# Kernel tuning notes

Hardware: AMD Instinct MI355X
Metric: run time of the kernel (lower is better)

## Reference

```python
import jax, jax.numpy as jnp
import numpy as np

HEADS = 4
DIM_U = 1
DIM_K = 16
DIM_V = 32  # dim_out // heads = 128 // 4
EPS = 1e-5


def setup_inputs() -> dict:
    key = jax.random.key(0)
    ks = jax.random.split(key, 9)
    b, dim, hh, ww = 16, 256, 32, 32
    n = m = hh * ww
    x = jax.random.normal(ks[0], (b, dim, hh, ww), dtype=jnp.float32)
    # 1x1 conv weights (out_ch, in_ch), kaiming-ish scale
    s = 1.0 / np.sqrt(dim)
    w_q = jax.random.normal(ks[1], (DIM_K * HEADS, dim), dtype=jnp.float32) * s
    w_k = jax.random.normal(ks[2], (DIM_K * DIM_U, dim), dtype=jnp.float32) * s
    w_v = jax.random.normal(ks[3], (DIM_V * DIM_U, dim), dtype=jnp.float32) * s
    pos_emb = jax.random.normal(ks[4], (n, m, DIM_K, DIM_U), dtype=jnp.float32)
    gamma_q = jnp.ones((DIM_K * HEADS,), dtype=jnp.float32)
    beta_q = jnp.zeros((DIM_K * HEADS,), dtype=jnp.float32)
    gamma_v = jnp.ones((DIM_V * DIM_U,), dtype=jnp.float32)
    beta_v = jnp.zeros((DIM_V * DIM_U,), dtype=jnp.float32)
    return {"x": x, "w_q": w_q, "w_k": w_k, "w_v": w_v, "pos_emb": pos_emb,
            "gamma_q": gamma_q, "beta_q": beta_q, "gamma_v": gamma_v, "beta_v": beta_v}


def _bn(t, gamma, beta):
    # BatchNorm2d in training mode: batch statistics over (b, h, w), biased var
    mean = t.mean(axis=(0, 2, 3), keepdims=True)
    var = t.var(axis=(0, 2, 3), keepdims=True)
    t = (t - mean) * jax.lax.rsqrt(var + EPS)
    return t * gamma[None, :, None, None] + beta[None, :, None, None]


def reference(x, w_q, w_k, w_v, pos_emb, gamma_q, beta_q, gamma_v, beta_v):
    b, c, hh, ww = x.shape
    h, u, dk, dv = HEADS, DIM_U, DIM_K, DIM_V
    # 1x1 convs == channel contractions
    q = jnp.einsum('oc,bcxy->boxy', w_q, x)
    k = jnp.einsum('oc,bcxy->boxy', w_k, x)
    v = jnp.einsum('oc,bcxy->boxy', w_v, x)
    q = _bn(q, gamma_q, beta_q)
    v = _bn(v, gamma_v, beta_v)
    n = hh * ww
    q = q.reshape(b, h, dk, n)        # b h k n
    k = k.reshape(b, dk, u, n)        # b k u m
    v = v.reshape(b, dv, u, n)        # b v u m
    k = jax.nn.softmax(k, axis=-1)
    lam_c = jnp.einsum('bkum,bvum->bkv', k, v)            # content lambda
    lam_p = jnp.einsum('nmku,bvum->bnkv', pos_emb, v)     # position lambdas
    Yc = jnp.einsum('bhkn,bkv->bnhv', q, lam_c)
    Yp = jnp.einsum('bhkn,bnkv->bnhv', q, lam_p)
    Y = Yc + Yp                                           # b n h v
    out = Y.transpose(0, 2, 3, 1).reshape(b, h * dv, hh, ww)
    return out
```

## Files before the change

### kernel.cpp

```cpp
#include <hip/hip_runtime.h>
#include <hip/hip_bf16.h>
#include <cstdint>


typedef __attribute__((ext_vector_type(8))) __bf16 bf16x8;
typedef __attribute__((ext_vector_type(4))) float f32x4;

__device__ __forceinline__ unsigned short f2bf(float f) {
    unsigned u = __float_as_uint(f);
    u += 0x7fffu + ((u >> 16) & 1u);
    return (unsigned short)(u >> 16);
}
__device__ __forceinline__ float bf2f(unsigned short h) {
    return __uint_as_float(((unsigned)h) << 16);
}
__device__ __forceinline__ void async16(const void* g, void* l) {
    __builtin_amdgcn_global_load_lds(
        (const __attribute__((address_space(1))) void*)g,
        (__attribute__((address_space(3))) void*)l, 16, 0, 0);
}

__global__ __launch_bounds__(256) void k_transp(const float* __restrict__ pos,
                                                unsigned* __restrict__ PbfU,
                                                const float* __restrict__ wq,
                                                const float* __restrict__ wk,
                                                const float* __restrict__ wv,
                                                unsigned* __restrict__ WbfU) {
    int blk = blockIdx.x;
    int t = threadIdx.x;
    if (blk >= 1024) {
        int tt = (blk - 1024) * 256 + t;
#pragma unroll
        for (int r = 0; r < 4; ++r) {
            int u = r * 4096 + tt;
            int row = u >> 7;
            int cp = (u & 127) << 1;
            float f0 = 0.f, f1 = 0.f;
            if (row < 64)       { f0 = wq[row * 256 + cp];        f1 = wq[row * 256 + cp + 1]; }
            else if (row < 80)  { f0 = wk[(row - 64) * 256 + cp]; f1 = wk[(row - 64) * 256 + cp + 1]; }
            else if (row < 112) { f0 = wv[(row - 80) * 256 + cp]; f1 = wv[(row - 80) * 256 + cp + 1]; }
            WbfU[u] = (unsigned)f2bf(f0) | ((unsigned)f2bf(f1) << 16);
        }
        return;
    }
    __shared__ __align__(16) unsigned short L[16 * 1032];
    const float4* src = (const float4*)(pos + (size_t)blk * 16384);
#pragma unroll
    for (int r = 0; r < 16; ++r) {
        int idx4 = r * 256 + t;
        float4 f = src[idx4];
        int m = idx4 >> 2, k0 = (idx4 & 3) << 2;
        L[(k0 + 0) * 1032 + m] = f2bf(f.x);
        L[(k0 + 1) * 1032 + m] = f2bf(f.y);
        L[(k0 + 2) * 1032 + m] = f2bf(f.z);
        L[(k0 + 3) * 1032 + m] = f2bf(f.w);
    }
    __syncthreads();
    uint2* dst = (uint2*)(PbfU + (size_t)blk * 8192);
#pragma unroll
    for (int r = 0; r < 16; ++r) {
        int c = r * 256 + t;
        int k = c >> 8, mo = c & 255;
        dst[c] = *(const uint2*)&L[k * 1032 + mo * 4];
    }
}

__global__ __launch_bounds__(256) void k_proj(const float* __restrict__ x,
                                              const unsigned short* __restrict__ Wbf,
                                              float* __restrict__ qraw,
                                              float* __restrict__ kraw,
                                              float* __restrict__ vraw) {
    int b = blockIdx.y;
    int px0 = blockIdx.x * 128;
    int t = threadIdx.x;
    int w = t >> 6, lane = t & 63;

    __shared__ __align__(16) unsigned short Al[128 * 32];
    __shared__ __align__(16) unsigned short Bl[128 * 40];

    int srow = (w << 5) + (lane >> 2);
    int schunk = (lane & 3) ^ ((lane >> 3) & 3);
    const unsigned short* pA0 = Wbf + srow * 256 + schunk * 8;
    const unsigned short* pA1 = pA0 + 16 * 256;
    unsigned short* lA0 = &Al[w * 1024];
    unsigned short* lA1 = lA0 + 512;

    int wm = w >> 1, wn = w & 1;
    int rl = lane & 15, qq = lane >> 4;
    int sw = qq ^ ((rl >> 1) & 3);

    f32x4 acc[4][4];
#pragma unroll
    for (int i = 0; i < 4; ++i)
#pragma unroll
        for (int j = 0; j < 4; ++j)
#pragma unroll
            for (int r = 0; r < 4; ++r) acc[i][j][r] = 0.f;

    const float* xb = x + (size_t)b * 256 * 1024 + px0;

    for (int kt = 0; kt < 8; ++kt) {
        int c0 = kt * 32;
        async16(pA0 + c0, lA0);
        async16(pA1 + c0, lA1);
#pragma unroll
        for (int rep = 0; rep < 8; ++rep) {
            int idx = rep * 256 + t;
            int px = idx & 127;
            int cp = idx >> 7;
            int c = c0 + cp * 2;
            float f0 = xb[(size_t)c * 1024 + px];
            float f1 = xb[(size_t)(c + 1) * 1024 + px];
            *(unsigned*)&Bl[px * 40 + cp * 2] = (unsigned)f2bf(f0) | ((unsigned)f2bf(f1) << 16);
        }
        __syncthreads();
        bf16x8 a[4], bb[4];
#pragma unroll
        for (int i = 0; i < 4; ++i) a[i]  = *(const bf16x8*)&Al[((wm << 6) + (i << 4) + rl) * 32 + sw * 8];
#pragma unroll
        for (int j = 0; j < 4; ++j) bb[j] = *(const bf16x8*)&Bl[((wn << 6) + (j << 4) + rl) * 40 + qq * 8];
#pragma unroll
        for (int i = 0; i < 4; ++i)
#pragma unroll
            for (int j = 0; j < 4; ++j)
                acc[i][j] = __builtin_amdgcn_mfma_f32_16x16x32_bf16(a[i], bb[j], acc[i][j], 0, 0, 0);
        __syncthreads();
    }

#pragma unroll
    for (int i = 0; i < 4; ++i) {
#pragma unroll
        for (int j = 0; j < 4; ++j) {
            int px = px0 + (wn << 6) + (j << 4) + (lane & 15);
#pragma unroll
            for (int r = 0; r < 4; ++r) {
                int ch = (wm << 6) + (i << 4) + ((lane >> 4) << 2) + r;
                float val = acc[i][j][r];
                if (ch < 64)       qraw[((size_t)b * 64 + ch) * 1024 + px] = val;
                else if (ch < 80)  kraw[((size_t)b * 16 + (ch - 64)) * 1024 + px] = val;
                else if (ch < 112) vraw[((size_t)b * 32 + (ch - 80)) * 1024 + px] = val;
            }
        }
    }
}

__global__ __launch_bounds__(1024) void k_stats(const float* __restrict__ qraw,
                                                const float* __restrict__ vraw,
                                                const float* __restrict__ gq, const float* __restrict__ bq,
                                                const float* __restrict__ gv, const float* __restrict__ bv,
                                                float* __restrict__ scaleArr, float* __restrict__ shiftArr) {
    int ch = blockIdx.x;
    int t = threadIdx.x;
    const float* base;
    size_t bstride;
    if (ch < 64) { base = qraw + (size_t)ch * 1024; bstride = 64 * 1024; }
    else         { base = vraw + (size_t)(ch - 64) * 1024; bstride = 32 * 1024; }
    float s = 0.f, ss = 0.f;
#pragma unroll
    for (int b = 0; b < 16; ++b) { float v = base[b * bstride + t]; s += v; ss += v * v; }
#pragma unroll
    for (int off = 32; off; off >>= 1) { s += __shfl_down(s, off); ss += __shfl_down(ss, off); }
    __shared__ float rs[16], rss[16];
    if ((t & 63) == 0) { rs[t >> 6] = s; rss[t >> 6] = ss; }
    __syncthreads();
    if (t == 0) {
        s = 0.f; ss = 0.f;
#pragma unroll
        for (int i = 0; i < 16; ++i) { s += rs[i]; ss += rss[i]; }
        float mean = s * (1.f / 16384.f);
        float var = ss * (1.f / 16384.f) - mean * mean;
        float g, be;
        if (ch < 64) { g = gq[ch]; be = bq[ch]; } else { g = gv[ch - 64]; be = bv[ch - 64]; }
        float sc = g * rsqrtf(var + 1e-5f);
        scaleArr[ch] = sc;
        shiftArr[ch] = be - mean * sc;
    }
}

__global__ void k_bn(const float* __restrict__ qraw, const float* __restrict__ vraw,
                     const float* __restrict__ scaleArr, const float* __restrict__ shiftArr,
                     float* __restrict__ qbn, unsigned* __restrict__ vbnU) {
    int bx = blockIdx.x;
    int t = threadIdx.x;
    if (bx < 256) {
        int nt = bx & 15, b = bx >> 4;
        __shared__ float Q[64 * 65];
        const float* src = qraw + (size_t)b * 64 * 1024 + nt * 64;
#pragma unroll
        for (int r = 0; r < 16; ++r) {
            int idx = r * 256 + t; int ch = idx >> 6; int nl = idx & 63;
            Q[ch * 65 + nl] = src[(size_t)ch * 1024 + nl];
        }
        __syncthreads();
        float* dst = qbn + ((size_t)b * 1024 + nt * 64) * 64;
#pragma unroll
        for (int r = 0; r < 16; ++r) {
            int idx = r * 256 + t; int nl = idx >> 6; int ch = idx & 63;
            dst[(size_t)nl * 64 + ch] = Q[ch * 65 + nl] * scaleArr[ch] + shiftArr[ch];
        }
    } else {
        int tt = (bx - 256) * 256 + t;
#pragma unroll
        for (int r = 0; r < 4; ++r) {
            int u = r * 65536 + tt;
            int row = u >> 9;
            int vch = row & 31;
            float sc = scaleArr[64 + vch], sh = shiftArr[64 + vch];
            float f0 = vraw[2 * u] * sc + sh;
            float f1 = vraw[2 * u + 1] * sc + sh;
            vbnU[u] = (unsigned)f2bf(f0) | ((unsigned)f2bf(f1) << 16);
        }
    }
}

__global__ void k_sm_lamc(const float* __restrict__ kraw, const unsigned short* __restrict__ vbn,
                          float* __restrict__ lamc) {
    int kch = blockIdx.x, b = blockIdx.y;
    int t = threadIdx.x; int w = t >> 6; int lane = t & 63;
    const float* kr = kraw + ((size_t)b * 16 + kch) * 1024;
    float xv[4];
    float mx = -1e30f;
#pragma unroll
    for (int i = 0; i < 4; ++i) { xv[i] = kr[t + i * 256]; mx = fmaxf(mx, xv[i]); }
#pragma unroll
    for (int off = 32; off; off >>= 1) mx = fmaxf(mx, __shfl_down(mx, off));
    __shared__ float red[4];
    __shared__ float pr[4][32];
    if (lane == 0) red[w] = mx;
    __syncthreads();
    mx = fmaxf(fmaxf(red[0], red[1]), fmaxf(red[2], red[3]));
    float e[4]; float s = 0.f;
#pragma unroll
    for (int i = 0; i < 4; ++i) { e[i] = __expf(xv[i] - mx); s += e[i]; }
#pragma unroll
    for (int off = 32; off; off >>= 1) s += __shfl_down(s, off);
    __syncthreads();
    if (lane == 0) red[w] = s;
    __syncthreads();
    float inv = 1.f / (red[0] + red[1] + red[2] + red[3]);
    const unsigned short* vb = vbn + (size_t)b * 32 * 1024;
    for (int vch = 0; vch < 32; ++vch) {
        const unsigned short* vr = vb + (size_t)vch * 1024;
        float p = 0.f;
#pragma unroll
        for (int i = 0; i < 4; ++i) p += e[i] * bf2f(vr[t + i * 256]);
#pragma unroll
        for (int off = 32; off; off >>= 1) p += __shfl_down(p, off);
        if (lane == 0) pr[w][vch] = p;
    }
    __syncthreads();
    if (t < 32) {
        float tot = pr[0][t] + pr[1][t] + pr[2][t] + pr[3][t];
        lamc[((size_t)b * 16 + kch) * 32 + t] = inv * tot;
    }
}

__global__ __launch_bounds__(256) void k_lamp(const unsigned short* __restrict__ Pbf,
                                              const unsigned short* __restrict__ vbn,
                                              const float* __restrict__ qbn,
                                              const float* __restrict__ lamc,
                                              float* __restrict__ out) {
    int mtile = blockIdx.x;
    int ntile = blockIdx.y;
    int t = threadIdx.x;
    int w = t >> 6, lane = t & 63;

    __shared__ union {
        __align__(16) unsigned short st[4][8192];
        float Y[128 * 128];
    } sm;

    int roff = lane >> 3;
    int jx = (lane & 7) ^ (roff & 7);
    const unsigned short* pA[4];
    const unsigned short* pB[4];
#pragma unroll
    for (int i = 0; i < 4; ++i) {
        int rowA = mtile * 128 + w * 32 + i * 8 + roff;
        int rowB = ntile * 128 + w * 32 + i * 8 + roff;
        pA[i] = Pbf + (size_t)rowA * 1024 + jx * 8;
        pB[i] = vbn + (size_t)rowB * 1024 + jx * 8;
    }

    int wm = w >> 1, wn = w & 1;
    int rl = lane & 15, qq = lane >> 4;
    int aoff[2][4], boff[2][4];
#pragma unroll
    for (int ks = 0; ks < 2; ++ks)
#pragma unroll
        for (int i = 0; i < 4; ++i) {
            int rowA = wm * 64 + i * 16 + rl;
            aoff[ks][i] = rowA * 64 + (((ks * 4 + qq) ^ (rowA & 7)) << 3);
            int rowB = wn * 64 + i * 16 + rl;
            boff[ks][i] = rowB * 64 + (((ks * 4 + qq) ^ (rowB & 7)) << 3);
        }

    f32x4 acc[4][4];
#pragma unroll
    for (int i = 0; i < 4; ++i)
#pragma unroll
        for (int j = 0; j < 4; ++j)
#pragma unroll
            for (int r = 0; r < 4; ++r) acc[i][j][r] = 0.f;

    auto stage = [&](unsigned short* dstA, int kk) {
        unsigned short* dstB = dstA + 8192;
#pragma unroll
        for (int i = 0; i < 4; ++i) {
            async16(pA[i] + kk * 64, dstA + w * 2048 + i * 512);
            async16(pB[i] + kk * 64, dstB + w * 2048 + i * 512);
        }
    };

    stage(sm.st[0], 0);
    __syncthreads();

    for (int kt = 0; kt < 16; ++kt) {
        unsigned short* curA = sm.st[(kt & 1) ? 2 : 0];
        unsigned short* curB = curA + 8192;
        if (kt < 15) stage(sm.st[(kt & 1) ? 0 : 2], kt + 1);
#pragma unroll
        for (int ks = 0; ks < 2; ++ks) {
            bf16x8 a[4], bb[4];
#pragma unroll
            for (int i = 0; i < 4; ++i) a[i]  = *(const bf16x8*)&curA[aoff[ks][i]];
#pragma unroll
            for (int j = 0; j < 4; ++j) bb[j] = *(const bf16x8*)&curB[boff[ks][j]];
#pragma unroll
            for (int i = 0; i < 4; ++i)
#pragma unroll
                for (int j = 0; j < 4; ++j)
                    acc[i][j] = __builtin_amdgcn_mfma_f32_16x16x32_bf16(a[i], bb[j], acc[i][j], 0, 0, 0);
        }
        __syncthreads();
    }

    int b0 = ntile * 4;
#pragma unroll
    for (int i = 0; i < 4; ++i) {
        int row_b = (wm << 6) + (i << 4) + ((lane >> 4) << 2);
#pragma unroll
        for (int j = 0; j < 4; ++j) {
            int col = (wn << 6) + (j << 4) + (lane & 15);
            int bcol = col >> 5, vv = col & 31;
            const float* lc = lamc + ((size_t)(b0 + bcol) * 16) * 32 + vv;
#pragma unroll
            for (int r = 0; r < 4; ++r) {
                int row = row_b + r;
                sm.Y[row * 128 + col] = acc[i][j][r] + lc[(row & 15) * 32];
            }
        }
    }
    __syncthreads();

    int c0 = t * 2;
    int bb2 = c0 >> 7;
    int hh = (c0 >> 5) & 3;
    int v0 = c0 & 31;
    int bglob = b0 + bb2;
    float o0[8], o1[8];
#pragma unroll
    for (int nn = 0; nn < 8; ++nn) { o0[nn] = 0.f; o1[nn] = 0.f; }
    const float* qb = qbn + ((size_t)bglob * 1024 + mtile * 8) * 64 + hh * 16;
#pragma unroll
    for (int nn = 0; nn < 8; ++nn) {
        const float* qr = qb + nn * 64;
        float qv[16];
        *(float4*)&qv[0]  = *(const float4*)&qr[0];
        *(float4*)&qv[4]  = *(const float4*)&qr[4];
        *(float4*)&qv[8]  = *(const float4*)&qr[8];
        *(float4*)&qv[12] = *(const float4*)&qr[12];
        const float* yrow = &sm.Y[(nn * 16) * 128 + bb2 * 32 + v0];
#pragma unroll
        for (int k = 0; k < 16; ++k) {
            float y0 = yrow[k * 128];
            float y1 = yrow[k * 128 + 1];
            o0[nn] += qv[k] * y0;
            o1[nn] += qv[k] * y1;
        }
    }
    float* op = out + ((size_t)bglob * 128 + hh * 32 + v0) * 1024 + mtile * 8;
    ((float4*)op)[0] = make_float4(o0[0], o0[1], o0[2], o0[3]);
    ((float4*)op)[1] = make_float4(o0[4], o0[5], o0[6], o0[7]);
    float* op1 = op + 1024;
    ((float4*)op1)[0] = make_float4(o1[0], o1[1], o1[2], o1[3]);
    ((float4*)op1)[1] = make_float4(o1[4], o1[5], o1[6], o1[7]);
}

extern "C" void kernel_launch(void* const* d_in, const int* in_sizes, int n_in,
                              void* d_out, int out_size, void* d_ws, size_t ws_size,
                              hipStream_t stream) {
    const float* x   = (const float*)d_in[0];
    const float* wq  = (const float*)d_in[1];
    const float* wk  = (const float*)d_in[2];
    const float* wv  = (const float*)d_in[3];
    const float* pos = (const float*)d_in[4];
    const float* gq  = (const float*)d_in[5];
    const float* bq  = (const float*)d_in[6];
    const float* gv  = (const float*)d_in[7];
    const float* bv  = (const float*)d_in[8];
    float* out = (float*)d_out;

    char* ws = (char*)d_ws;
    unsigned short* Pbf  = (unsigned short*)(ws);
    unsigned short* Wbf  = (unsigned short*)(ws + 33554432);
    float* qraw          = (float*)(ws + 33619968);
    float* kraw          = (float*)(ws + 37814272);
    float* vraw          = (float*)(ws + 38862848);
    float* qbn           = (float*)(ws + 40960000);
    unsigned short* vbn  = (unsigned short*)(ws + 45154304);
    float* scaleArr      = (float*)(ws + 46202880);
    float* shiftArr      = (float*)(ws + 46203392);
    float* lamc          = (float*)(ws + 46203904);

    k_transp<<<dim3(1040), dim3(256), 0, stream>>>(pos, (unsigned*)Pbf, wq, wk, wv, (unsigned*)Wbf);
    k_proj<<<dim3(8, 16), dim3(256), 0, stream>>>(x, Wbf, qraw, kraw, vraw);
    k_stats<<<dim3(96), dim3(1024), 0, stream>>>(qraw, vraw, gq, bq, gv, bv, scaleArr, shiftArr);
    k_bn<<<dim3(512), dim3(256), 0, stream>>>(qraw, vraw, scaleArr, shiftArr, qbn, (unsigned*)vbn);
    k_sm_lamc<<<dim3(16, 16), dim3(256), 0, stream>>>(kraw, vbn, lamc);
    k_lamp<<<dim3(128, 4), dim3(256), 0, stream>>>(Pbf, vbn, qbn, lamc, out);
}
```

Measured before the change: 198.4 us.

## Cut k_lamp LDS to single buffer with bf16 Y staging, halve proj tile

```diff
diff --git a/kernel.cpp b/kernel.cpp
--- a/kernel.cpp
+++ b/kernel.cpp
@@ -71,12 +71,12 @@
                                               float* __restrict__ kraw,
                                               float* __restrict__ vraw) {
     int b = blockIdx.y;
-    int px0 = blockIdx.x * 128;
+    int px0 = blockIdx.x * 64;
     int t = threadIdx.x;
     int w = t >> 6, lane = t & 63;
 
     __shared__ __align__(16) unsigned short Al[128 * 32];
-    __shared__ __align__(16) unsigned short Bl[128 * 40];
+    __shared__ __align__(16) unsigned short Bl[64 * 34];
 
     int srow = (w << 5) + (lane >> 2);
     int schunk = (lane & 3) ^ ((lane >> 3) & 3);
@@ -89,11 +89,11 @@
     int rl = lane & 15, qq = lane >> 4;
     int sw = qq ^ ((rl >> 1) & 3);
 
-    f32x4 acc[4][4];
+    f32x4 acc[4][2];
 #pragma unroll
     for (int i = 0; i < 4; ++i)
 #pragma unroll
-        for (int j = 0; j < 4; ++j)
+        for (int j = 0; j < 2; ++j)
 #pragma unroll
             for (int r = 0; r < 4; ++r) acc[i][j][r] = 0.f;
 
@@ -104,25 +104,25 @@
         async16(pA0 + c0, lA0);
         async16(pA1 + c0, lA1);
 #pragma unroll
-        for (int rep = 0; rep < 8; ++rep) {
+        for (int rep = 0; rep < 4; ++rep) {
             int idx = rep * 256 + t;
-            int px = idx & 127;
-            int cp = idx >> 7;
+            int px = idx & 63;
+            int cp = idx >> 6;
             int c = c0 + cp * 2;
             float f0 = xb[(size_t)c * 1024 + px];
             float f1 = xb[(size_t)(c + 1) * 1024 + px];
-            *(unsigned*)&Bl[px * 40 + cp * 2] = (unsigned)f2bf(f0) | ((unsigned)f2bf(f1) << 16);
+            *(unsigned*)&Bl[px * 34 + cp * 2] = (unsigned)f2bf(f0) | ((unsigned)f2bf(f1) << 16);
         }
         __syncthreads();
-        bf16x8 a[4], bb[4];
+        bf16x8 a[4], bb[2];
 #pragma unroll
         for (int i = 0; i < 4; ++i) a[i]  = *(const bf16x8*)&Al[((wm << 6) + (i << 4) + rl) * 32 + sw * 8];
 #pragma unroll
-        for (int j = 0; j < 4; ++j) bb[j] = *(const bf16x8*)&Bl[((wn << 6) + (j << 4) + rl) * 40 + qq * 8];
+        for (int j = 0; j < 2; ++j) bb[j] = *(const bf16x8*)&Bl[((wn << 5) + (j << 4) + rl) * 34 + qq * 8];
 #pragma unroll
         for (int i = 0; i < 4; ++i)
 #pragma unroll
-            for (int j = 0; j < 4; ++j)
+            for (int j = 0; j < 2; ++j)
                 acc[i][j] = __builtin_amdgcn_mfma_f32_16x16x32_bf16(a[i], bb[j], acc[i][j], 0, 0, 0);
         __syncthreads();
     }
@@ -130,8 +130,8 @@
 #pragma unroll
     for (int i = 0; i < 4; ++i) {
 #pragma unroll
-        for (int j = 0; j < 4; ++j) {
-            int px = px0 + (wn << 6) + (j << 4) + (lane & 15);
+        for (int j = 0; j < 2; ++j) {
+            int px = px0 + (wn << 5) + (j << 4) + (lane & 15);
 #pragma unroll
             for (int r = 0; r < 4; ++r) {
                 int ch = (wm << 6) + (i << 4) + ((lane >> 4) << 2) + r;
@@ -255,77 +255,60 @@
     }
 }
 
-__global__ __launch_bounds__(256) void k_lamp(const unsigned short* __restrict__ Pbf,
-                                              const unsigned short* __restrict__ vbn,
-                                              const float* __restrict__ qbn,
-                                              const float* __restrict__ lamc,
-                                              float* __restrict__ out) {
+__global__ __launch_bounds__(256, 4) void k_lamp(const unsigned short* __restrict__ Pbf,
+                                                 const unsigned short* __restrict__ vbn,
+                                                 const float* __restrict__ qbn,
+                                                 const float* __restrict__ lamc,
+                                                 float* __restrict__ out) {
     int mtile = blockIdx.x;
     int ntile = blockIdx.y;
     int t = threadIdx.x;
     int w = t >> 6, lane = t & 63;
 
     __shared__ union {
-        __align__(16) unsigned short st[4][8192];
-        float Y[128 * 128];
+        struct { __align__(16) unsigned short A[8192]; __align__(16) unsigned short B[8192]; } st;
+        unsigned short Ybf[128 * 132];
     } sm;
 
-    int roff = lane >> 3;
-    int jx = (lane & 7) ^ (roff & 7);
-    const unsigned short* pA[4];
-    const unsigned short* pB[4];
-#pragma unroll
-    for (int i = 0; i < 4; ++i) {
-        int rowA = mtile * 128 + w * 32 + i * 8 + roff;
-        int rowB = ntile * 128 + w * 32 + i * 8 + roff;
-        pA[i] = Pbf + (size_t)rowA * 1024 + jx * 8;
-        pB[i] = vbn + (size_t)rowB * 1024 + jx * 8;
-    }
+    int srow = t >> 3;
+    int jx = (t & 7) ^ (srow & 7);
+    const unsigned short* pA = Pbf + ((size_t)(mtile * 128) + srow) * 1024 + jx * 8;
+    const unsigned short* pB = vbn + ((size_t)(ntile * 128) + srow) * 1024 + jx * 8;
+    unsigned short* ldsA = &sm.st.A[t * 8];
+    unsigned short* ldsB = &sm.st.B[t * 8];
 
     int wm = w >> 1, wn = w & 1;
     int rl = lane & 15, qq = lane >> 4;
-    int aoff[2][4], boff[2][4];
-#pragma unroll
-    for (int ks = 0; ks < 2; ++ks)
+    int abase[2], bbase[2];
+#pragma unroll
+    for (int ks = 0; ks < 2; ++ks) {
+        abase[ks] = (wm * 64 + rl) * 64 + (((ks * 4 + qq) ^ (rl & 7)) << 3);
+        bbase[ks] = (wn * 64 + rl) * 64 + (((ks * 4 + qq) ^ (rl & 7)) << 3);
+    }
+
+    f32x4 acc[4][4];
+#pragma unroll
+    for (int i = 0; i < 4; ++i)
+#pragma unroll
+        for (int j = 0; j < 4; ++j)
+#pragma unroll
+            for (int r = 0; r < 4; ++r) acc[i][j][r] = 0.f;
+
+    for (int kt = 0; kt < 16; ++kt) {
+        int m0 = kt * 64;
 #pragma unroll
         for (int i = 0; i < 4; ++i) {
-            int rowA = wm * 64 + i * 16 + rl;
-            aoff[ks][i] = rowA * 64 + (((ks * 4 + qq) ^ (rowA & 7)) << 3);
-            int rowB = wn * 64 + i * 16 + rl;
-            boff[ks][i] = rowB * 64 + (((ks * 4 + qq) ^ (rowB & 7)) << 3);
-        }
-
-    f32x4 acc[4][4];
-#pragma unroll
-    for (int i = 0; i < 4; ++i)
-#pragma unroll
-        for (int j = 0; j < 4; ++j)
-#pragma unroll
-            for (int r = 0; r < 4; ++r) acc[i][j][r] = 0.f;
-
-    auto stage = [&](unsigned short* dstA, int kk) {
-        unsigned short* dstB = dstA + 8192;
-#pragma unroll
-        for (int i = 0; i < 4; ++i) {
-            async16(pA[i] + kk * 64, dstA + w * 2048 + i * 512);
-            async16(pB[i] + kk * 64, dstB + w * 2048 + i * 512);
-        }
-    };
-
-    stage(sm.st[0], 0);
-    __syncthreads();
-
-    for (int kt = 0; kt < 16; ++kt) {
-        unsigned short* curA = sm.st[(kt & 1) ? 2 : 0];
-        unsigned short* curB = curA + 8192;
-        if (kt < 15) stage(sm.st[(kt & 1) ? 0 : 2], kt + 1);
+            async16(pA + (size_t)i * 32 * 1024 + m0, ldsA + i * 2048);
+            async16(pB + (size_t)i * 32 * 1024 + m0, ldsB + i * 2048);
+        }
+        __syncthreads();
 #pragma unroll
         for (int ks = 0; ks < 2; ++ks) {
             bf16x8 a[4], bb[4];
 #pragma unroll
-            for (int i = 0; i < 4; ++i) a[i]  = *(const bf16x8*)&curA[aoff[ks][i]];
-#pragma unroll
-            for (int j = 0; j < 4; ++j) bb[j] = *(const bf16x8*)&curB[boff[ks][j]];
+            for (int i = 0; i < 4; ++i) a[i]  = *(const bf16x8*)&sm.st.A[abase[ks] + i * 1024];
+#pragma unroll
+            for (int j = 0; j < 4; ++j) bb[j] = *(const bf16x8*)&sm.st.B[bbase[ks] + j * 1024];
 #pragma unroll
             for (int i = 0; i < 4; ++i)
 #pragma unroll
@@ -338,16 +321,16 @@
     int b0 = ntile * 4;
 #pragma unroll
     for (int i = 0; i < 4; ++i) {
-        int row_b = (wm << 6) + (i << 4) + ((lane >> 4) << 2);
+        int row_b = (wm << 6) + (i << 4) + (qq << 2);
 #pragma unroll
         for (int j = 0; j < 4; ++j) {
-            int col = (wn << 6) + (j << 4) + (lane & 15);
+            int col = (wn << 6) + (j << 4) + rl;
             int bcol = col >> 5, vv = col & 31;
             const float* lc = lamc + ((size_t)(b0 + bcol) * 16) * 32 + vv;
 #pragma unroll
             for (int r = 0; r < 4; ++r) {
                 int row = row_b + r;
-                sm.Y[row * 128 + col] = acc[i][j][r] + lc[(row & 15) * 32];
+                sm.Ybf[row * 132 + col] = f2bf(acc[i][j][r] + lc[(row & 15) * 32]);
             }
         }
     }
@@ -370,11 +353,11 @@
         *(float4*)&qv[4]  = *(const float4*)&qr[4];
         *(float4*)&qv[8]  = *(const float4*)&qr[8];
         *(float4*)&qv[12] = *(const float4*)&qr[12];
-        const float* yrow = &sm.Y[(nn * 16) * 128 + bb2 * 32 + v0];
+        const unsigned short* yrow = &sm.Ybf[(nn * 16) * 132 + bb2 * 32 + v0];
 #pragma unroll
         for (int k = 0; k < 16; ++k) {
-            float y0 = yrow[k * 128];
-            float y1 = yrow[k * 128 + 1];
+            float y0 = bf2f(yrow[k * 132]);
+            float y1 = bf2f(yrow[k * 132 + 1]);
             o0[nn] += qv[k] * y0;
             o1[nn] += qv[k] * y1;
         }
@@ -414,7 +397,7 @@
     float* lamc          = (float*)(ws + 46203904);
 
     k_transp<<<dim3(1040), dim3(256), 0, stream>>>(pos, (unsigned*)Pbf, wq, wk, wv, (unsigned*)Wbf);
-    k_proj<<<dim3(8, 16), dim3(256), 0, stream>>>(x, Wbf, qraw, kraw, vraw);
+    k_proj<<<dim3(16, 16), dim3(256), 0, stream>>>(x, Wbf, qraw, kraw, vraw);
     k_stats<<<dim3(96), dim3(1024), 0, stream>>>(qraw, vraw, gq, bq, gv, bv, scaleArr, shiftArr);
     k_bn<<<dim3(512), dim3(256), 0, stream>>>(qraw, vraw, scaleArr, shiftArr, qbn, (unsigned*)vbn);
     k_sm_lamc<<<dim3(16, 16), dim3(256), 0, stream>>>(kraw, vbn, lamc);
```

Result: faster. 188.7 us (-4.9%).
